# Performance work log

Hardware: AMD Instinct MI355X
Metric: run time of the kernel (lower is better)

## Reference

```python
import jax, jax.numpy as jnp
import numpy as np

THRESHOLD_LOWER = 1.0  # 'highly_nonlinear' group curvature threshold


def _menger_curvature(target):
    # target: [T, N, 2] -> curvature at each interior point: [T-2, N]
    p0, p1, p2 = target[:-2], target[1:-1], target[2:]
    area_twice = jnp.abs(
        p0[..., 0] * (p1[..., 1] - p2[..., 1])
        + p1[..., 0] * (p2[..., 1] - p0[..., 1])
        + p2[..., 0] * (p0[..., 1] - p1[..., 1])
    )
    dist = (
        jnp.linalg.norm(p1 - p0, axis=-1)
        * jnp.linalg.norm(p2 - p1, axis=-1)
        * jnp.linalg.norm(p2 - p0, axis=-1)
    )
    k = 2.0 * area_twice / dist
    return jnp.where(jnp.isnan(k), 0.0, k)  # k[k != k] = 0


def _max_run_length(mask):
    # mask: [T-2, N] float {0,1}. Longest run of consecutive 1s per pedestrian.
    def step(carry, m):
        run, mx = carry
        run = run + m               # increment where mask==1 (unchanged where 0)
        mx = jnp.maximum(mx, run)   # matches both branches of the torch loop
        run = run * m               # reset run where mask==0
        return (run, mx), None
    n = mask.shape[1]
    init = (jnp.zeros((n,), mask.dtype), jnp.zeros((n,), mask.dtype))
    (_, mx), _ = jax.lax.scan(step, init, mask)
    return mx


def setup_inputs() -> dict:
    key = jax.random.key(0)
    k1, k2 = jax.random.split(key)
    T, N = 12, 1_500_000
    inp = jax.random.normal(k1, (T, N, 2), dtype=jnp.float32)
    tgt = jax.random.normal(k2, (T, N, 2), dtype=jnp.float32)
    return {"input": inp, "target": tgt}


def reference(input, target):
    curv = _menger_curvature(target)                     # [T-2, N]
    mask = (jnp.abs(curv) >= THRESHOLD_LOWER).astype(curv.dtype)
    max_entries = _max_run_length(mask)                  # [N]
    sum_mask = mask.sum(axis=0)                          # [N]
    criteria = (max_entries >= 3.0) & (max_entries < 11.0) & (sum_mask > 0.0)
    sel = criteria.astype(input.dtype)
    # ADE per pedestrian on selected (highly nonlinear) trajectories
    ade = jnp.linalg.norm(input - target, axis=-1).mean(axis=0)  # [N]
    cnt = sel.sum()
    loss = jnp.where(cnt > 0.0, jnp.sum(ade * sel) / jnp.maximum(cnt, 1.0), 0.0)
    return loss
```

## Files before the change

### kernel.cpp

```cpp
#include <hip/hip_runtime.h>
#include <math.h>

#define T_DIM 12
#define GRID_BLOCKS 2048

__global__ __launch_bounds__(256) void ade_traj_kernel(
    const float4* __restrict__ inp,
    const float4* __restrict__ tgt,
    int npairs,
    float2* __restrict__ partials)
{
    const int stride = gridDim.x * blockDim.x;
    float num = 0.0f;
    float cnt = 0.0f;

    for (int i = blockIdx.x * blockDim.x + threadIdx.x; i < npairs; i += stride) {
        float ade_a = 0.0f, ade_b = 0.0f;
        float run_a = 0.0f, mx_a = 0.0f, sm_a = 0.0f;
        float run_b = 0.0f, mx_b = 0.0f, sm_b = 0.0f;
        float p0ax = 0.f, p0ay = 0.f, p1ax = 0.f, p1ay = 0.f;
        float p0bx = 0.f, p0by = 0.f, p1bx = 0.f, p1by = 0.f;

        #pragma unroll
        for (int t = 0; t < T_DIM; ++t) {
            const int off = t * npairs + i;
            float4 tv = tgt[off];
            float4 iv = inp[off];

            {
                float dx = iv.x - tv.x, dy = iv.y - tv.y;
                ade_a += __builtin_amdgcn_sqrtf(dx * dx + dy * dy);
                float dxb = iv.z - tv.z, dyb = iv.w - tv.w;
                ade_b += __builtin_amdgcn_sqrtf(dxb * dxb + dyb * dyb);
            }

            if (t >= 2) {
                {
                    float cx = tv.x, cy = tv.y;
                    float ar = p0ax * (p1ay - cy) + p1ax * (cy - p0ay) + cx * (p0ay - p1ay);
                    float a2 = 4.0f * ar * ar;
                    float ex, ey;
                    ex = p1ax - p0ax; ey = p1ay - p0ay; float e01 = ex * ex + ey * ey;
                    ex = cx - p1ax;   ey = cy - p1ay;   float e12 = ex * ex + ey * ey;
                    ex = cx - p0ax;   ey = cy - p0ay;   float e02 = ex * ex + ey * ey;
                    float d2 = e01 * e12 * e02;
                    float m = ((a2 >= d2) && !(d2 == 0.0f && a2 == 0.0f)) ? 1.0f : 0.0f;
                    run_a += m;
                    mx_a = fmaxf(mx_a, run_a);
                    run_a *= m;
                    sm_a += m;
                }
                {
                    float cx = tv.z, cy = tv.w;
                    float ar = p0bx * (p1by - cy) + p1bx * (cy - p0by) + cx * (p0by - p1by);
                    float a2 = 4.0f * ar * ar;
                    float ex, ey;
                    ex = p1bx - p0bx; ey = p1by - p0by; float e01 = ex * ex + ey * ey;
                    ex = cx - p1bx;   ey = cy - p1by;   float e12 = ex * ex + ey * ey;
                    ex = cx - p0bx;   ey = cy - p0by;   float e02 = ex * ex + ey * ey;
                    float d2 = e01 * e12 * e02;
                    float m = ((a2 >= d2) && !(d2 == 0.0f && a2 == 0.0f)) ? 1.0f : 0.0f;
                    run_b += m;
                    mx_b = fmaxf(mx_b, run_b);
                    run_b *= m;
                    sm_b += m;
                }
            }
            p0ax = p1ax; p0ay = p1ay; p1ax = tv.x; p1ay = tv.y;
            p0bx = p1bx; p0by = p1by; p1bx = tv.z; p1by = tv.w;
        }

        bool sel_a = (mx_a >= 3.0f) && (sm_a > 0.0f);
        bool sel_b = (mx_b >= 3.0f) && (sm_b > 0.0f);
        if (sel_a) { num += ade_a * (1.0f / 12.0f); cnt += 1.0f; }
        if (sel_b) { num += ade_b * (1.0f / 12.0f); cnt += 1.0f; }
    }

    #pragma unroll
    for (int off = 32; off > 0; off >>= 1) {
        num += __shfl_down(num, off, 64);
        cnt += __shfl_down(cnt, off, 64);
    }

    __shared__ float snum[4], scnt[4];
    const int wave = threadIdx.x >> 6;
    const int lane = threadIdx.x & 63;
    if (lane == 0) { snum[wave] = num; scnt[wave] = cnt; }
    __syncthreads();
    if (threadIdx.x == 0) {
        float n = 0.0f, c = 0.0f;
        #pragma unroll
        for (int w = 0; w < 4; ++w) { n += snum[w]; c += scnt[w]; }
        partials[blockIdx.x] = make_float2(n, c);
    }
}

__global__ __launch_bounds__(256) void ade_traj_finalize(
    const float2* __restrict__ partials, int g, float* __restrict__ out)
{
    float n = 0.0f, c = 0.0f;
    for (int j = threadIdx.x; j < g; j += 256) {
        float2 p = partials[j];
        n += p.x; c += p.y;
    }
    #pragma unroll
    for (int off = 32; off > 0; off >>= 1) {
        n += __shfl_down(n, off, 64);
        c += __shfl_down(c, off, 64);
    }
    __shared__ float sn[4], sc[4];
    const int wave = threadIdx.x >> 6;
    const int lane = threadIdx.x & 63;
    if (lane == 0) { sn[wave] = n; sc[wave] = c; }
    __syncthreads();
    if (threadIdx.x == 0) {
        float ns = 0.0f, cs = 0.0f;
        #pragma unroll
        for (int w = 0; w < 4; ++w) { ns += sn[w]; cs += sc[w]; }
        out[0] = (cs > 0.0f) ? (ns / fmaxf(cs, 1.0f)) : 0.0f;
    }
}

extern "C" void kernel_launch(void* const* d_in, const int* in_sizes, int n_in,
                              void* d_out, int out_size, void* d_ws, size_t ws_size,
                              hipStream_t stream) {
    const float* inp = (const float*)d_in[0];
    const float* tgt = (const float*)d_in[1];
    float* out = (float*)d_out;
    float2* partials = (float2*)d_ws;

    const int total = in_sizes[0];
    const int N = total / (T_DIM * 2);
    const int npairs = N / 2;

    ade_traj_kernel<<<GRID_BLOCKS, 256, 0, stream>>>(
        (const float4*)inp, (const float4*)tgt, npairs, partials);
    ade_traj_finalize<<<1, 256, 0, stream>>>(partials, GRID_BLOCKS, out);
}
```

Measured before the change: 52.85 us.

## Batch all timestep loads up front and halve the grid with occupancy bounds

Each thread now loads all 12 target and 12 input float4 values into registers before doing any math. A sched_barrier keeps the compiler from interleaving these loads with the compute, which raises memory-level parallelism for this bandwidth-bound streaming kernel. The grid is halved to 1024 blocks and launch bounds ask for 4 blocks per CU. In exchange it uses many more VGPRs (96 for the loaded data alone), which can lower occupancy, and the smaller grid may leave the memory system less saturated.

Result: slower. 92.79 us (+75.6%).

```diff
diff --git a/kernel.cpp b/kernel.cpp
--- a/kernel.cpp
+++ b/kernel.cpp
@@ -2,9 +2,9 @@
 #include <math.h>
 
 #define T_DIM 12
-#define GRID_BLOCKS 2048
+#define GRID_BLOCKS 1024
 
-__global__ __launch_bounds__(256) void ade_traj_kernel(
+__global__ __launch_bounds__(256, 4) void ade_traj_kernel(
     const float4* __restrict__ inp,
     const float4* __restrict__ tgt,
     int npairs,
@@ -15,59 +15,61 @@
     float cnt = 0.0f;
 
     for (int i = blockIdx.x * blockDim.x + threadIdx.x; i < npairs; i += stride) {
+        float4 tv[T_DIM];
+        float4 iv[T_DIM];
+        #pragma unroll
+        for (int t = 0; t < T_DIM; ++t) tv[t] = tgt[t * npairs + i];
+        #pragma unroll
+        for (int t = 0; t < T_DIM; ++t) iv[t] = inp[t * npairs + i];
+        __builtin_amdgcn_sched_barrier(0);
+
         float ade_a = 0.0f, ade_b = 0.0f;
+        #pragma unroll
+        for (int t = 0; t < T_DIM; ++t) {
+            float dx = iv[t].x - tv[t].x, dy = iv[t].y - tv[t].y;
+            ade_a += __builtin_amdgcn_sqrtf(dx * dx + dy * dy);
+            float dxb = iv[t].z - tv[t].z, dyb = iv[t].w - tv[t].w;
+            ade_b += __builtin_amdgcn_sqrtf(dxb * dxb + dyb * dyb);
+        }
+
         float run_a = 0.0f, mx_a = 0.0f, sm_a = 0.0f;
         float run_b = 0.0f, mx_b = 0.0f, sm_b = 0.0f;
-        float p0ax = 0.f, p0ay = 0.f, p1ax = 0.f, p1ay = 0.f;
-        float p0bx = 0.f, p0by = 0.f, p1bx = 0.f, p1by = 0.f;
-
         #pragma unroll
-        for (int t = 0; t < T_DIM; ++t) {
-            const int off = t * npairs + i;
-            float4 tv = tgt[off];
-            float4 iv = inp[off];
-
+        for (int t = 2; t < T_DIM; ++t) {
             {
-                float dx = iv.x - tv.x, dy = iv.y - tv.y;
-                ade_a += __builtin_amdgcn_sqrtf(dx * dx + dy * dy);
-                float dxb = iv.z - tv.z, dyb = iv.w - tv.w;
-                ade_b += __builtin_amdgcn_sqrtf(dxb * dxb + dyb * dyb);
+                float ax = tv[t-2].x, ay = tv[t-2].y;
+                float bx = tv[t-1].x, by = tv[t-1].y;
+                float cx = tv[t].x,   cy = tv[t].y;
+                float ar = ax * (by - cy) + bx * (cy - ay) + cx * (ay - by);
+                float a2 = 4.0f * ar * ar;
+                float ex, ey;
+                ex = bx - ax; ey = by - ay; float e01 = ex * ex + ey * ey;
+                ex = cx - bx; ey = cy - by; float e12 = ex * ex + ey * ey;
+                ex = cx - ax; ey = cy - ay; float e02 = ex * ex + ey * ey;
+                float d2 = e01 * e12 * e02;
+                float m = ((a2 >= d2) && !(d2 == 0.0f && a2 == 0.0f)) ? 1.0f : 0.0f;
+                run_a += m;
+                mx_a = fmaxf(mx_a, run_a);
+                run_a *= m;
+                sm_a += m;
             }
-
-            if (t >= 2) {
-                {
-                    float cx = tv.x, cy = tv.y;
-                    float ar = p0ax * (p1ay - cy) + p1ax * (cy - p0ay) + cx * (p0ay - p1ay);
-                    float a2 = 4.0f * ar * ar;
-                    float ex, ey;
-                    ex = p1ax - p0ax; ey = p1ay - p0ay; float e01 = ex * ex + ey * ey;
-                    ex = cx - p1ax;   ey = cy - p1ay;   float e12 = ex * ex + ey * ey;
-                    ex = cx - p0ax;   ey = cy - p0ay;   float e02 = ex * ex + ey * ey;
-                    float d2 = e01 * e12 * e02;
-                    float m = ((a2 >= d2) && !(d2 == 0.0f && a2 == 0.0f)) ? 1.0f : 0.0f;
-                    run_a += m;
-                    mx_a = fmaxf(mx_a, run_a);
-                    run_a *= m;
-                    sm_a += m;
-                }
-                {
-                    float cx = tv.z, cy = tv.w;
-                    float ar = p0bx * (p1by - cy) + p1bx * (cy - p0by) + cx * (p0by - p1by);
-                    float a2 = 4.0f * ar * ar;
-                    float ex, ey;
-                    ex = p1bx - p0bx; ey = p1by - p0by; float e01 = ex * ex + ey * ey;
-                    ex = cx - p1bx;   ey = cy - p1by;   float e12 = ex * ex + ey * ey;
-                    ex = cx - p0bx;   ey = cy - p0by;   float e02 = ex * ex + ey * ey;
-                    float d2 = e01 * e12 * e02;
-                    float m = ((a2 >= d2) && !(d2 == 0.0f && a2 == 0.0f)) ? 1.0f : 0.0f;
-                    run_b += m;
-                    mx_b = fmaxf(mx_b, run_b);
-                    run_b *= m;
-                    sm_b += m;
-                }
+            {
+                float ax = tv[t-2].z, ay = tv[t-2].w;
+                float bx = tv[t-1].z, by = tv[t-1].w;
+                float cx = tv[t].z,   cy = tv[t].w;
+                float ar = ax * (by - cy) + bx * (cy - ay) + cx * (ay - by);
+                float a2 = 4.0f * ar * ar;
+                float ex, ey;
+                ex = bx - ax; ey = by - ay; float e01 = ex * ex + ey * ey;
+                ex = cx - bx; ey = cy - by; float e12 = ex * ex + ey * ey;
+                ex = cx - ax; ey = cy - ay; float e02 = ex * ex + ey * ey;
+                float d2 = e01 * e12 * e02;
+                float m = ((a2 >= d2) && !(d2 == 0.0f && a2 == 0.0f)) ? 1.0f : 0.0f;
+                run_b += m;
+                mx_b = fmaxf(mx_b, run_b);
+                run_b *= m;
+                sm_b += m;
             }
-            p0ax = p1ax; p0ay = p1ay; p1ax = tv.x; p1ay = tv.y;
-            p0bx = p1bx; p0by = p1by; p1bx = tv.z; p1by = tv.w;
         }
 
         bool sel_a = (mx_a >= 3.0f) && (sm_a > 0.0f);
```
